# Optimization experiments

Hardware: AMD Instinct MI355X
Metric: run time of the kernel (lower is better)

Reference implementation:

```python
import jax, jax.numpy as jnp
import numpy as np

B, C, H, W = 8, 256, 64, 64


def setup_inputs() -> dict:
    key = jax.random.key(0)
    ks = jax.random.split(key, 8)
    s = 1.0 / np.sqrt(C)
    return {
        "x": jax.random.normal(ks[0], (B, C, H, W), dtype=jnp.float32),
        "Wq": jax.random.normal(ks[1], (C, C), dtype=jnp.float32) * s,
        "bq": jax.random.normal(ks[2], (C,), dtype=jnp.float32) * 0.01,
        "Wk": jax.random.normal(ks[3], (C, C), dtype=jnp.float32) * s,
        "bk": jax.random.normal(ks[4], (C,), dtype=jnp.float32) * 0.01,
        "Wv": jax.random.normal(ks[5], (C, C), dtype=jnp.float32) * s,
        "bv": jax.random.normal(ks[6], (C,), dtype=jnp.float32) * 0.01,
        "gamma": jax.random.normal(ks[7], (1,), dtype=jnp.float32) * 0.1,
    }


def reference(x, Wq, bq, Wk, bk, Wv, bv, gamma):
    b, c, h, w = x.shape
    xf = x.reshape(b, c, h * w)                       # (B, C, N)
    # 1x1 conv == per-pixel linear: out_c = W @ in_c + bias
    q = jnp.einsum('oc,bcn->bon', Wq, xf) + bq[None, :, None]
    k = jnp.einsum('oc,bcn->bon', Wk, xf) + bk[None, :, None]
    v = jnp.einsum('oc,bcn->bon', Wv, xf) + bv[None, :, None]
    # attention_map[b, i, j] = sum_c q[b, c, i] * k[b, c, j]  (no scaling in original)
    scores = jnp.einsum('bci,bcj->bij', q, k)         # (B, N, N)
    attn = jax.nn.softmax(scores, axis=-1)
    # out[b, c, i] = sum_j v[b, c, j] * attn[b, i, j]
    out = jnp.einsum('bcj,bij->bci', v, attn)
    out = out.reshape(b, c, h, w)
    return x + gamma[0] * out
```

## Files before the change

kernel.cpp:

```cpp
#include <hip/hip_runtime.h>

#define BATCH 8
#define CCH 256
#define NPOS 4096
#define LOG2E 1.4426950408889634f

typedef __bf16 bf16x8 __attribute__((ext_vector_type(8)));
typedef float f32x4 __attribute__((ext_vector_type(4)));
typedef int i32x4 __attribute__((ext_vector_type(4)));
typedef int i32x2 __attribute__((ext_vector_type(2)));

typedef const __attribute__((address_space(1))) void GAS;
typedef __attribute__((address_space(3))) void LAS;

#define CFENCE() __asm__ volatile("" ::: "memory")
#define WAIT_VM8()  do { CFENCE(); __builtin_amdgcn_s_waitcnt(0x0F78); CFENCE(); } while (0)
#define WAIT_LGKM0() do { CFENCE(); __builtin_amdgcn_s_waitcnt(0xC07F); CFENCE(); } while (0)
#define BAR_RAW() do { CFENCE(); __builtin_amdgcn_s_barrier(); CFENCE(); } while (0)

__device__ __forceinline__ unsigned short f2bf(float f) {
  unsigned u = __builtin_bit_cast(unsigned, f);
  u += 0x7fffu + ((u >> 16) & 1u);
  return (unsigned short)(u >> 16);
}

__device__ __forceinline__ bf16x8 ld_bf8(const unsigned short* p) {
  i32x4 t = *reinterpret_cast<const i32x4*>(p);
  return __builtin_bit_cast(bf16x8, t);
}

__device__ __forceinline__ float fexp2(float x) {
#if __has_builtin(__builtin_amdgcn_exp2f)
  return __builtin_amdgcn_exp2f(x);
#else
  return __builtin_exp2f(x);
#endif
}

__device__ __forceinline__ unsigned cvtpk(float lo, float hi) {
  unsigned r;
  asm("v_cvt_pk_bf16_f32 %0, %1, %2" : "=v"(r) : "v"(lo), "v"(hi));
  return r;
}

__global__ void cvt_kernel(const float* __restrict__ Wq,
                           const float* __restrict__ Wk,
                           const float* __restrict__ Wv,
                           unsigned short* __restrict__ dst)
{
  const int idx = blockIdx.x * 256 + threadIdx.x;
  const float* src = (idx < 65536) ? Wq : ((idx < 131072) ? Wk : Wv);
  dst[idx] = f2bf(src[idx & 65535]);
}

__global__ __launch_bounds__(256, 3)
void qkv_kernel(const float* __restrict__ x,
                const unsigned short* __restrict__ Wall,
                const float* __restrict__ bq,
                const float* __restrict__ bk,
                const float* __restrict__ bv,
                unsigned short* __restrict__ qT,
                unsigned short* __restrict__ kT,
                unsigned short* __restrict__ vG)
{
  __shared__ __align__(16) unsigned short xT[64 * 264];
  __shared__ __align__(16) unsigned short tbuf[64 * 72];

  const int b   = blockIdx.x;
  const int i0  = blockIdx.y * 64;
  const int tid = threadIdx.x;
  const int w   = tid >> 6;
  const int l   = tid & 63;
  const int n   = l & 15;
  const int q4  = l >> 4;

  {
    const int li = tid & 15;
    const int cg = tid >> 4;
#pragma unroll
    for (int it = 0; it < 16; ++it) {
      const int c = it * 16 + cg;
      f32x4 f = *reinterpret_cast<const f32x4*>(x + ((size_t)b * CCH + c) * NPOS + i0 + li * 4);
#pragma unroll
      for (int e = 0; e < 4; ++e) xT[(li * 4 + e) * 264 + c] = f2bf(f[e]);
    }
  }
  __syncthreads();

  const size_t qbase = (size_t)b * NPOS * CCH;
  bool first = true;

  for (int s = 0; s < 3; ++s) {
    const float* bias = (s == 0) ? bq : (s == 1) ? bk : bv;
    for (int op = 0; op < 4; ++op) {
      const int obase = op * 64;

      const unsigned short* Wp = Wall + s * 65536 + (size_t)(obase + w * 16 + n) * CCH + q4 * 8;
      bf16x8 wfr[8];
#pragma unroll
      for (int kk = 0; kk < 8; ++kk) wfr[kk] = ld_bf8(Wp + kk * 32);

      float bo[4];
#pragma unroll
      for (int r = 0; r < 4; ++r) bo[r] = bias[obase + w * 16 + q4 * 4 + r];

      f32x4 acc[4];
#pragma unroll
      for (int pt = 0; pt < 4; ++pt) {
        acc[pt] = {0.f, 0.f, 0.f, 0.f};
#pragma unroll
        for (int kk = 0; kk < 8; ++kk) {
          bf16x8 bfr = ld_bf8(&xT[(pt * 16 + n) * 264 + kk * 32 + q4 * 8]);
          acc[pt] = __builtin_amdgcn_mfma_f32_16x16x32_bf16(wfr[kk], bfr, acc[pt], 0, 0, 0);
        }
      }

      if (!first) __syncthreads();
      first = false;
      if (s < 2) {
        const float sc = (s == 0) ? LOG2E : 1.0f;
#pragma unroll
        for (int pt = 0; pt < 4; ++pt)
#pragma unroll
          for (int r = 0; r < 4; ++r)
            tbuf[(pt * 16 + n) * 72 + w * 16 + q4 * 4 + r] = f2bf((acc[pt][r] + bo[r]) * sc);
      } else {
#pragma unroll
        for (int pt = 0; pt < 4; ++pt)
#pragma unroll
          for (int r = 0; r < 4; ++r)
            tbuf[(w * 16 + q4 * 4 + r) * 72 + pt * 16 + n] = f2bf(acc[pt][r] + bo[r]);
      }
      __syncthreads();

      if (s < 2) {
        unsigned short* dst = (s == 0 ? qT : kT) + qbase;
#pragma unroll
        for (int it2 = 0; it2 < 2; ++it2) {
          const int idx = it2 * 256 + tid;
          const int pos = idx >> 3, ow = (idx & 7) * 8;
          i32x4 d = *reinterpret_cast<const i32x4*>(&tbuf[pos * 72 + ow]);
          *reinterpret_cast<i32x4*>(&dst[(size_t)(i0 + pos) * CCH + obase + ow]) = d;
        }
      } else {
#pragma unroll
        for (int it2 = 0; it2 < 2; ++it2) {
          const int idx = it2 * 256 + tid;
          const int o = idx >> 3, pw2 = (idx & 7) * 8;
          i32x4 d = *reinterpret_cast<const i32x4*>(&tbuf[o * 72 + pw2]);
          *reinterpret_cast<i32x4*>(&vG[qbase + (size_t)(obase + o) * NPOS + i0 + pw2]) = d;
        }
      }
    }
  }
}

__global__ __launch_bounds__(256, 2)
void attn_kernel(const unsigned short* __restrict__ qT,
                 const unsigned short* __restrict__ kT,
                 const unsigned short* __restrict__ vG,
                 const float* __restrict__ x,
                 const float* __restrict__ gamma,
                 float* __restrict__ out)
{
  __shared__ __align__(16) unsigned short kbuf[2][64 * 256];
  __shared__ __align__(16) unsigned short pbuf[64 * 64];
  __shared__ float stat_lds[64];

  const int b   = blockIdx.x;
  const int i0  = blockIdx.y * 64;
  const int tid = threadIdx.x;
  const int w   = tid >> 6;
  const int l   = tid & 63;
  const int n   = l & 15;
  const int q4  = l >> 4;
  const int nsw = n & 7;

  const unsigned short* qTb = qT + (size_t)b * NPOS * CCH;
  const unsigned short* kTb = kT + (size_t)b * NPOS * CCH;
  const unsigned short* vb  = vG + (size_t)b * NPOS * CCH;

  bf16x8 afr[8];
  {
    const unsigned short* qrow = qTb + (size_t)(i0 + w * 16 + n) * CCH + q4 * 8;
#pragma unroll
    for (int kk = 0; kk < 8; ++kk)
      afr[kk] = ld_bf8(qrow + kk * 32);
  }

  {
#pragma unroll
    for (int it = 0; it < 8; ++it) {
      const int t = w * 8 + it;
      const int j = 2 * t + (l >> 5);
      const int gp = l & 31;
      const int g  = gp ^ (j & 7);
      const unsigned short* src = kTb + (size_t)j * CCH + g * 8;
      unsigned short* dst = &kbuf[0][t * 512];
      __builtin_amdgcn_global_load_lds((GAS*)src, (LAS*)dst, 16, 0, 0);
    }
  }

  f32x4 O[16];
#pragma unroll
  for (int t = 0; t < 16; ++t) O[t] = {0.f, 0.f, 0.f, 0.f};
  float mcur = 64.f;
  float lrow = 0.f;
  float acarry = 1.0f;

  for (int jt = 0; jt < 64; ++jt) {
    const int j0 = jt * 64;
    const unsigned short* kb = kbuf[jt & 1];

    i32x4 vreg[8];
#pragma unroll
    for (int ct = 0; ct < 4; ++ct) {
      const unsigned short* vp = vb + (size_t)(w * 64 + ct * 16 + n) * NPOS + j0 + q4 * 8;
      vreg[ct * 2]     = *reinterpret_cast<const i32x4*>(vp);
      vreg[ct * 2 + 1] = *reinterpret_cast<const i32x4*>(vp + 32);
    }

    WAIT_VM8();
    BAR_RAW();

    f32x4 sacc[4];
    __builtin_amdgcn_s_setprio(1);
#pragma unroll
    for (int nt = 0; nt < 4; ++nt) {
      const unsigned short* krow = kb + (nt * 16 + n) * 256;
      sacc[nt] = {0.f, 0.f, 0.f, 0.f};
#pragma unroll
      for (int kk = 0; kk < 8; ++kk) {
        const int gp = (kk * 4 + q4) ^ nsw;
        bf16x8 bfr = ld_bf8(krow + gp * 8);
        sacc[nt] = __builtin_amdgcn_mfma_f32_16x16x32_bf16(bfr, afr[kk], sacc[nt], 0, 0, 0);
      }
    }
    __builtin_amdgcn_s_setprio(0);

    float tml;
    {
      float a0 = fmaxf(fmaxf(sacc[0][0], sacc[0][1]), fmaxf(sacc[0][2], sacc[0][3]));
      float a1 = fmaxf(fmaxf(sacc[1][0], sacc[1][1]), fmaxf(sacc[1][2], sacc[1][3]));
      float a2 = fmaxf(fmaxf(sacc[2][0], sacc[2][1]), fmaxf(sacc[2][2], sacc[2][3]));
      float a3 = fmaxf(fmaxf(sacc[3][0], sacc[3][1]), fmaxf(sacc[3][2], sacc[3][3]));
      tml = fmaxf(fmaxf(a0, a1), fmaxf(a2, a3));
    }

    float s = 0.f;
#pragma unroll
    for (int nt = 0; nt < 4; ++nt) {
#pragma unroll
      for (int r = 0; r < 4; ++r) {
        const float p = fexp2(sacc[nt][r] - mcur);
        sacc[nt][r] = p;
        s += p;
      }
    }

    {
      const int rowb = (w * 16 + n) * 64;
#pragma unroll
      for (int nt = 0; nt < 4; ++nt) {
        const unsigned lo = cvtpk(sacc[nt][0], sacc[nt][1]);
        const unsigned hi = cvtpk(sacc[nt][2], sacc[nt][3]);
        const int pg = (2 * nt + (q4 >> 1)) ^ nsw;
        i32x2 dv = { (int)lo, (int)hi };
        *reinterpret_cast<i32x2*>(&pbuf[rowb + pg * 8 + (q4 & 1) * 4]) = dv;
      }
    }
    if (q4 == 0) stat_lds[w * 16 + n] = acarry;

    s += __shfl_xor(s, 16);
    s += __shfl_xor(s, 32);
    lrow += s;
    float tm = fmaxf(tml, __shfl_xor(tml, 16));
    tm = fmaxf(tm, __shfl_xor(tm, 32));

    {
      const int j0n = ((jt + 1) & 63) * 64;
      unsigned short* bufn = kbuf[(jt + 1) & 1];
#pragma unroll
      for (int it = 0; it < 8; ++it) {
        const int t = w * 8 + it;
        const int j = 2 * t + (l >> 5);
        const int gp = l & 31;
        const int g  = gp ^ (j & 7);
        const unsigned short* src = kTb + (size_t)(j0n + j) * CCH + g * 8;
        unsigned short* dst = &bufn[t * 512];
        __builtin_amdgcn_global_load_lds((GAS*)src, (LAS*)dst, 16, 0, 0);
      }
    }

    WAIT_LGKM0();
    BAR_RAW();

    {
      const float al0 = stat_lds[n];
      const float al1 = stat_lds[16 + n];
      const float al2 = stat_lds[32 + n];
      const float al3 = stat_lds[48 + n];
      if (al0 + al1 + al2 + al3 != 4.0f) {
        const float als[4] = { al0, al1, al2, al3 };
#pragma unroll
        for (int it = 0; it < 4; ++it) {
          const float al = als[it];
#pragma unroll
          for (int ct = 0; ct < 4; ++ct) {
            f32x4& o = O[ct * 4 + it];
            o[0] *= al; o[1] *= al; o[2] *= al; o[3] *= al;
          }
        }
      }
    }

    bf16x8 pf[8];
#pragma unroll
    for (int it = 0; it < 4; ++it) {
      const int rowb = (it * 16 + n) * 64;
      pf[it * 2 + 0] = ld_bf8(&pbuf[rowb + ((q4 ^ nsw) << 3)]);
      pf[it * 2 + 1] = ld_bf8(&pbuf[rowb + (((4 + q4) ^ nsw) << 3)]);
    }
    __builtin_amdgcn_s_setprio(1);
#pragma unroll
    for (int ct = 0; ct < 4; ++ct) {
      bf16x8 vf0 = __builtin_bit_cast(bf16x8, vreg[ct * 2]);
      bf16x8 vf1 = __builtin_bit_cast(bf16x8, vreg[ct * 2 + 1]);
#pragma unroll
      for (int it = 0; it < 4; ++it) {
        O[ct * 4 + it] = __builtin_amdgcn_mfma_f32_16x16x32_bf16(vf0, pf[it * 2 + 0], O[ct * 4 + it], 0, 0, 0);
        O[ct * 4 + it] = __builtin_amdgcn_mfma_f32_16x16x32_bf16(vf1, pf[it * 2 + 1], O[ct * 4 + it], 0, 0, 0);
      }
    }
    __builtin_amdgcn_s_setprio(0);

    const int upd = tm > mcur + 8.f;
    if (__any(upd)) {
      const float mn = upd ? tm : mcur;
      const float al = fexp2(mcur - mn);
      mcur = mn;
      lrow *= al;
      acarry = al;
    } else {
      acarry = 1.0f;
    }
  }

  __syncthreads();
  if (q4 == 0) stat_lds[w * 16 + n] = acarry / lrow;
  __syncthreads();

  const float g = gamma[0];
#pragma unroll
  for (int it = 0; it < 4; ++it) {
    const float sc = g * stat_lds[it * 16 + n];
    const int ipos = i0 + it * 16 + n;
#pragma unroll
    for (int ct = 0; ct < 4; ++ct) {
#pragma unroll
      for (int r = 0; r < 4; ++r) {
        const int c = w * 64 + ct * 16 + q4 * 4 + r;
        const size_t idx = ((size_t)(b * CCH + c)) * NPOS + ipos;
        out[idx] = x[idx] + sc * O[ct * 4 + it][r];
      }
    }
  }
}

extern "C" void kernel_launch(void* const* d_in, const int* in_sizes, int n_in,
                              void* d_out, int out_size, void* d_ws, size_t ws_size,
                              hipStream_t stream)
{
  const float* x     = (const float*)d_in[0];
  const float* Wq    = (const float*)d_in[1];
  const float* bq    = (const float*)d_in[2];
  const float* Wk    = (const float*)d_in[3];
  const float* bk    = (const float*)d_in[4];
  const float* Wv    = (const float*)d_in[5];
  const float* bv    = (const float*)d_in[6];
  const float* gamma = (const float*)d_in[7];
  float* out = (float*)d_out;

  unsigned short* ws   = (unsigned short*)d_ws;
  unsigned short* Wall = ws;
  unsigned short* qT   = ws + 196608;
  unsigned short* kT   = qT + (size_t)BATCH * NPOS * CCH;
  unsigned short* vG   = kT + (size_t)BATCH * NPOS * CCH;

  cvt_kernel<<<768, 256, 0, stream>>>(Wq, Wk, Wv, Wall);
  qkv_kernel<<<dim3(8, 64), 256, 0, stream>>>(x, Wall, bq, bk, bv, qT, kT, vG);
  attn_kernel<<<dim3(8, 64), 256, 0, stream>>>(qT, kT, vG, x, gamma, out);
}
```

Before: 296.1 us.

## Split QK^T work so each wave computes two query groups over half the keys

Each of the four waves now owns two 16-row query groups and half of the 64-key tile, instead of one query group against all keys. Each K fragment read from LDS feeds two MFMAs, so LDS K reads per MFMA are halved. Partial row sums and maxima are exchanged between wave pairs through a new shared stats array. This costs more VGPRs, since two sets of Q fragments are held, and adds an extra LDS stat exchange. The launch bound is expressed as amdgpu_waves_per_eu(2,2).

```diff
diff --git a/kernel.cpp b/kernel.cpp
--- a/kernel.cpp
+++ b/kernel.cpp
@@ -155,7 +155,7 @@
   }
 }
 
-__global__ __launch_bounds__(256, 2)
+__global__ __launch_bounds__(256) __attribute__((amdgpu_waves_per_eu(2, 2)))
 void attn_kernel(const unsigned short* __restrict__ qT,
                  const unsigned short* __restrict__ kT,
                  const unsigned short* __restrict__ vG,
@@ -166,6 +166,7 @@
   __shared__ __align__(16) unsigned short kbuf[2][64 * 256];
   __shared__ __align__(16) unsigned short pbuf[64 * 64];
   __shared__ float stat_lds[64];
+  __shared__ float sstat[2][2][64];
 
   const int b   = blockIdx.x;
   const int i0  = blockIdx.y * 64;
@@ -175,17 +176,20 @@
   const int n   = l & 15;
   const int q4  = l >> 4;
   const int nsw = n & 7;
+  const int ip  = w >> 1;
+  const int jh  = w & 1;
 
   const unsigned short* qTb = qT + (size_t)b * NPOS * CCH;
   const unsigned short* kTb = kT + (size_t)b * NPOS * CCH;
   const unsigned short* vb  = vG + (size_t)b * NPOS * CCH;
 
-  bf16x8 afr[8];
-  {
-    const unsigned short* qrow = qTb + (size_t)(i0 + w * 16 + n) * CCH + q4 * 8;
+  bf16x8 afr[2][8];
+#pragma unroll
+  for (int ig = 0; ig < 2; ++ig) {
+    const unsigned short* qrow = qTb + (size_t)(i0 + (ip * 2 + ig) * 16 + n) * CCH + q4 * 8;
 #pragma unroll
     for (int kk = 0; kk < 8; ++kk)
-      afr[kk] = ld_bf8(qrow + kk * 32);
+      afr[ig][kk] = ld_bf8(qrow + kk * 32);
   }
 
   {
@@ -204,9 +208,9 @@
   f32x4 O[16];
 #pragma unroll
   for (int t = 0; t < 16; ++t) O[t] = {0.f, 0.f, 0.f, 0.f};
-  float mcur = 64.f;
-  float lrow = 0.f;
-  float acarry = 1.0f;
+  float mcur[2] = {64.f, 64.f};
+  float lrow[2] = {0.f, 0.f};
+  float acarry[2] = {1.0f, 1.0f};
 
   for (int jt = 0; jt < 64; ++jt) {
     const int j0 = jt * 64;
@@ -223,59 +227,73 @@
     WAIT_VM8();
     BAR_RAW();
 
-    f32x4 sacc[4];
+    f32x4 sacc[2][2];
+#pragma unroll
+    for (int nt2 = 0; nt2 < 2; ++nt2)
+#pragma unroll
+      for (int ig = 0; ig < 2; ++ig) sacc[nt2][ig] = {0.f, 0.f, 0.f, 0.f};
     __builtin_amdgcn_s_setprio(1);
 #pragma unroll
-    for (int nt = 0; nt < 4; ++nt) {
-      const unsigned short* krow = kb + (nt * 16 + n) * 256;
-      sacc[nt] = {0.f, 0.f, 0.f, 0.f};
+    for (int nt2 = 0; nt2 < 2; ++nt2) {
+      const unsigned short* krow = kb + (jh * 32 + nt2 * 16 + n) * 256;
 #pragma unroll
       for (int kk = 0; kk < 8; ++kk) {
         const int gp = (kk * 4 + q4) ^ nsw;
-        bf16x8 bfr = ld_bf8(krow + gp * 8);
-        sacc[nt] = __builtin_amdgcn_mfma_f32_16x16x32_bf16(bfr, afr[kk], sacc[nt], 0, 0, 0);
+        bf16x8 kfr = ld_bf8(krow + gp * 8);
+        sacc[nt2][0] = __builtin_amdgcn_mfma_f32_16x16x32_bf16(kfr, afr[0][kk], sacc[nt2][0], 0, 0, 0);
+        sacc[nt2][1] = __builtin_amdgcn_mfma_f32_16x16x32_bf16(kfr, afr[1][kk], sacc[nt2][1], 0, 0, 0);
       }
     }
     __builtin_amdgcn_s_setprio(0);
 
-    float tml;
-    {
-      float a0 = fmaxf(fmaxf(sacc[0][0], sacc[0][1]), fmaxf(sacc[0][2], sacc[0][3]));
-      float a1 = fmaxf(fmaxf(sacc[1][0], sacc[1][1]), fmaxf(sacc[1][2], sacc[1][3]));
-      float a2 = fmaxf(fmaxf(sacc[2][0], sacc[2][1]), fmaxf(sacc[2][2], sacc[2][3]));
-      float a3 = fmaxf(fmaxf(sacc[3][0], sacc[3][1]), fmaxf(sacc[3][2], sacc[3][3]));
-      tml = fmaxf(fmaxf(a0, a1), fmaxf(a2, a3));
-    }
-
-    float s = 0.f;
-#pragma unroll
-    for (int nt = 0; nt < 4; ++nt) {
-#pragma unroll
-      for (int r = 0; r < 4; ++r) {
-        const float p = fexp2(sacc[nt][r] - mcur);
-        sacc[nt][r] = p;
-        s += p;
-      }
-    }
-
-    {
-      const int rowb = (w * 16 + n) * 64;
-#pragma unroll
-      for (int nt = 0; nt < 4; ++nt) {
-        const unsigned lo = cvtpk(sacc[nt][0], sacc[nt][1]);
-        const unsigned hi = cvtpk(sacc[nt][2], sacc[nt][3]);
-        const int pg = (2 * nt + (q4 >> 1)) ^ nsw;
+    float tml[2], s_[2];
+#pragma unroll
+    for (int ig = 0; ig < 2; ++ig) {
+      float a0 = fmaxf(fmaxf(sacc[0][ig][0], sacc[0][ig][1]), fmaxf(sacc[0][ig][2], sacc[0][ig][3]));
+      float a1 = fmaxf(fmaxf(sacc[1][ig][0], sacc[1][ig][1]), fmaxf(sacc[1][ig][2], sacc[1][ig][3]));
+      tml[ig] = fmaxf(a0, a1);
+      float s = 0.f;
+#pragma unroll
+      for (int nt2 = 0; nt2 < 2; ++nt2)
+#pragma unroll
+        for (int r = 0; r < 4; ++r) {
+          const float p = fexp2(sacc[nt2][ig][r] - mcur[ig]);
+          sacc[nt2][ig][r] = p;
+          s += p;
+        }
+      s_[ig] = s;
+    }
+
+#pragma unroll
+    for (int ig = 0; ig < 2; ++ig) {
+      const int rowb = ((ip * 2 + ig) * 16 + n) * 64;
+#pragma unroll
+      for (int nt2 = 0; nt2 < 2; ++nt2) {
+        const unsigned lo = cvtpk(sacc[nt2][ig][0], sacc[nt2][ig][1]);
+        const unsigned hi = cvtpk(sacc[nt2][ig][2], sacc[nt2][ig][3]);
+        const int pg = (jh * 4 + nt2 * 2 + (q4 >> 1)) ^ nsw;
         i32x2 dv = { (int)lo, (int)hi };
         *reinterpret_cast<i32x2*>(&pbuf[rowb + pg * 8 + (q4 & 1) * 4]) = dv;
       }
     }
-    if (q4 == 0) stat_lds[w * 16 + n] = acarry;
-
-    s += __shfl_xor(s, 16);
-    s += __shfl_xor(s, 32);
-    lrow += s;
-    float tm = fmaxf(tml, __shfl_xor(tml, 16));
-    tm = fmaxf(tm, __shfl_xor(tm, 32));
+
+#pragma unroll
+    for (int ig = 0; ig < 2; ++ig) {
+      s_[ig] += __shfl_xor(s_[ig], 16);
+      s_[ig] += __shfl_xor(s_[ig], 32);
+      tml[ig] = fmaxf(tml[ig], __shfl_xor(tml[ig], 16));
+      tml[ig] = fmaxf(tml[ig], __shfl_xor(tml[ig], 32));
+    }
+
+    if (q4 == 0) {
+#pragma unroll
+      for (int ig = 0; ig < 2; ++ig) {
+        const int irow = (ip * 2 + ig) * 16 + n;
+        sstat[jh][0][irow] = s_[ig];
+        sstat[jh][1][irow] = tml[ig];
+        if (jh == 0) stat_lds[irow] = acarry[ig];
+      }
+    }
 
     {
       const int j0n = ((jt + 1) & 63) * 64;
@@ -295,6 +313,14 @@
     WAIT_LGKM0();
     BAR_RAW();
 
+    float sp[2], mp[2];
+#pragma unroll
+    for (int ig = 0; ig < 2; ++ig) {
+      const int irow = (ip * 2 + ig) * 16 + n;
+      sp[ig] = sstat[jh ^ 1][0][irow];
+      mp[ig] = sstat[jh ^ 1][1][irow];
+    }
+
     {
       const float al0 = stat_lds[n];
       const float al1 = stat_lds[16 + n];
@@ -334,20 +360,34 @@
     }
     __builtin_amdgcn_s_setprio(0);
 
-    const int upd = tm > mcur + 8.f;
-    if (__any(upd)) {
-      const float mn = upd ? tm : mcur;
-      const float al = fexp2(mcur - mn);
-      mcur = mn;
-      lrow *= al;
-      acarry = al;
+    const float tm0 = fmaxf(tml[0], mp[0]);
+    const float tm1 = fmaxf(tml[1], mp[1]);
+    lrow[0] += s_[0] + sp[0];
+    lrow[1] += s_[1] + sp[1];
+    const int upd0 = tm0 > mcur[0] + 8.f;
+    const int upd1 = tm1 > mcur[1] + 8.f;
+    if (__any(upd0 | upd1)) {
+      {
+        const float mn = upd0 ? tm0 : mcur[0];
+        const float al = fexp2(mcur[0] - mn);
+        mcur[0] = mn; lrow[0] *= al; acarry[0] = al;
+      }
+      {
+        const float mn = upd1 ? tm1 : mcur[1];
+        const float al = fexp2(mcur[1] - mn);
+        mcur[1] = mn; lrow[1] *= al; acarry[1] = al;
+      }
     } else {
-      acarry = 1.0f;
+      acarry[0] = 1.0f; acarry[1] = 1.0f;
     }
   }
 
   __syncthreads();
-  if (q4 == 0) stat_lds[w * 16 + n] = acarry / lrow;
+  if (q4 == 0 && jh == 0) {
+#pragma unroll
+    for (int ig = 0; ig < 2; ++ig)
+      stat_lds[(ip * 2 + ig) * 16 + n] = acarry[ig] / lrow[ig];
+  }
   __syncthreads();
 
   const float g = gamma[0];
```

Result: slower. 350.6 us (+18.4%).

## Double-buffer QKV staging tile and prefetch next weight fragments

Applied to the files above, without the earlier changes.

Flattens the QKV projection's 12 output phases into one fully unrolled loop. Each phase now prefetches the next phase's weight fragments and biases into registers while the current MFMAs run. The transpose staging buffer becomes double-buffered, so one of the two barriers per phase can be dropped. The aim is to hide global weight-load latency and reduce synchronisation, at the cost of more registers and LDS, which could lower occupancy under the launch bound of 3.

```diff
diff --git a/kernel.cpp b/kernel.cpp
--- a/kernel.cpp
+++ b/kernel.cpp
@@ -64,7 +64,7 @@
                 unsigned short* __restrict__ vG)
 {
   __shared__ __align__(16) unsigned short xT[64 * 264];
-  __shared__ __align__(16) unsigned short tbuf[64 * 72];
+  __shared__ __align__(16) unsigned short tbuf[2][64 * 72];
 
   const int b   = blockIdx.x;
   const int i0  = blockIdx.y * 64;
@@ -88,69 +88,87 @@
   __syncthreads();
 
   const size_t qbase = (size_t)b * NPOS * CCH;
-  bool first = true;
-
-  for (int s = 0; s < 3; ++s) {
-    const float* bias = (s == 0) ? bq : (s == 1) ? bk : bv;
-    for (int op = 0; op < 4; ++op) {
-      const int obase = op * 64;
-
-      const unsigned short* Wp = Wall + s * 65536 + (size_t)(obase + w * 16 + n) * CCH + q4 * 8;
-      bf16x8 wfr[8];
-#pragma unroll
-      for (int kk = 0; kk < 8; ++kk) wfr[kk] = ld_bf8(Wp + kk * 32);
-
-      float bo[4];
-#pragma unroll
-      for (int r = 0; r < 4; ++r) bo[r] = bias[obase + w * 16 + q4 * 4 + r];
-
-      f32x4 acc[4];
-#pragma unroll
-      for (int pt = 0; pt < 4; ++pt) {
-        acc[pt] = {0.f, 0.f, 0.f, 0.f};
-#pragma unroll
-        for (int kk = 0; kk < 8; ++kk) {
-          bf16x8 bfr = ld_bf8(&xT[(pt * 16 + n) * 264 + kk * 32 + q4 * 8]);
-          acc[pt] = __builtin_amdgcn_mfma_f32_16x16x32_bf16(wfr[kk], bfr, acc[pt], 0, 0, 0);
-        }
-      }
-
-      if (!first) __syncthreads();
-      first = false;
-      if (s < 2) {
-        const float sc = (s == 0) ? LOG2E : 1.0f;
-#pragma unroll
-        for (int pt = 0; pt < 4; ++pt)
-#pragma unroll
-          for (int r = 0; r < 4; ++r)
-            tbuf[(pt * 16 + n) * 72 + w * 16 + q4 * 4 + r] = f2bf((acc[pt][r] + bo[r]) * sc);
-      } else {
-#pragma unroll
-        for (int pt = 0; pt < 4; ++pt)
-#pragma unroll
-          for (int r = 0; r < 4; ++r)
-            tbuf[(w * 16 + q4 * 4 + r) * 72 + pt * 16 + n] = f2bf(acc[pt][r] + bo[r]);
-      }
-      __syncthreads();
-
-      if (s < 2) {
-        unsigned short* dst = (s == 0 ? qT : kT) + qbase;
-#pragma unroll
-        for (int it2 = 0; it2 < 2; ++it2) {
-          const int idx = it2 * 256 + tid;
-          const int pos = idx >> 3, ow = (idx & 7) * 8;
-          i32x4 d = *reinterpret_cast<const i32x4*>(&tbuf[pos * 72 + ow]);
-          *reinterpret_cast<i32x4*>(&dst[(size_t)(i0 + pos) * CCH + obase + ow]) = d;
-        }
-      } else {
-#pragma unroll
-        for (int it2 = 0; it2 < 2; ++it2) {
-          const int idx = it2 * 256 + tid;
-          const int o = idx >> 3, pw2 = (idx & 7) * 8;
-          i32x4 d = *reinterpret_cast<const i32x4*>(&tbuf[o * 72 + pw2]);
-          *reinterpret_cast<i32x4*>(&vG[qbase + (size_t)(obase + o) * NPOS + i0 + pw2]) = d;
-        }
-      }
+  const float* const biases[3] = { bq, bk, bv };
+
+  bf16x8 wcur[8];
+  float bcur[4];
+  {
+    const unsigned short* Wp = Wall + (size_t)(w * 16 + n) * CCH + q4 * 8;
+#pragma unroll
+    for (int kk = 0; kk < 8; ++kk) wcur[kk] = ld_bf8(Wp + kk * 32);
+#pragma unroll
+    for (int r = 0; r < 4; ++r) bcur[r] = bq[w * 16 + q4 * 4 + r];
+  }
+
+#pragma unroll
+  for (int ph = 0; ph < 12; ++ph) {
+    const int s = ph >> 2, op = ph & 3, obase = op * 64;
+
+    bf16x8 wnxt[8];
+    float bnxt[4];
+    if (ph < 11) {
+      const int s2 = (ph + 1) >> 2, op2 = (ph + 1) & 3;
+      const unsigned short* Wp =
+          Wall + s2 * 65536 + (size_t)(op2 * 64 + w * 16 + n) * CCH + q4 * 8;
+#pragma unroll
+      for (int kk = 0; kk < 8; ++kk) wnxt[kk] = ld_bf8(Wp + kk * 32);
+      const float* b2 = biases[s2];
+#pragma unroll
+      for (int r = 0; r < 4; ++r) bnxt[r] = b2[op2 * 64 + w * 16 + q4 * 4 + r];
+    }
+
+    f32x4 acc[4];
+#pragma unroll
+    for (int pt = 0; pt < 4; ++pt) {
+      acc[pt] = {0.f, 0.f, 0.f, 0.f};
+#pragma unroll
+      for (int kk = 0; kk < 8; ++kk) {
+        bf16x8 bfr = ld_bf8(&xT[(pt * 16 + n) * 264 + kk * 32 + q4 * 8]);
+        acc[pt] = __builtin_amdgcn_mfma_f32_16x16x32_bf16(wcur[kk], bfr, acc[pt], 0, 0, 0);
+      }
+    }
+
+    unsigned short* tb = tbuf[ph & 1];
+    if (s < 2) {
+      const float sc = (s == 0) ? LOG2E : 1.0f;
+#pragma unroll
+      for (int pt = 0; pt < 4; ++pt)
+#pragma unroll
+        for (int r = 0; r < 4; ++r)
+          tb[(pt * 16 + n) * 72 + w * 16 + q4 * 4 + r] = f2bf((acc[pt][r] + bcur[r]) * sc);
+    } else {
+#pragma unroll
+      for (int pt = 0; pt < 4; ++pt)
+#pragma unroll
+        for (int r = 0; r < 4; ++r)
+          tb[(w * 16 + q4 * 4 + r) * 72 + pt * 16 + n] = f2bf(acc[pt][r] + bcur[r]);
+    }
+    __syncthreads();
+
+    if (s < 2) {
+      unsigned short* dst = (s == 0 ? qT : kT) + qbase;
+#pragma unroll
+      for (int it2 = 0; it2 < 2; ++it2) {
+        const int idx = it2 * 256 + tid;
+        const int pos = idx >> 3, ow = (idx & 7) * 8;
+        i32x4 d = *reinterpret_cast<const i32x4*>(&tb[pos * 72 + ow]);
+        *reinterpret_cast<i32x4*>(&dst[(size_t)(i0 + pos) * CCH + obase + ow]) = d;
+      }
+    } else {
+#pragma unroll
+      for (int it2 = 0; it2 < 2; ++it2) {
+        const int idx = it2 * 256 + tid;
+        const int o = idx >> 3, pw2 = (idx & 7) * 8;
+        i32x4 d = *reinterpret_cast<const i32x4*>(&tb[o * 72 + pw2]);
+        *reinterpret_cast<i32x4*>(&vG[qbase + (size_t)(obase + o) * NPOS + i0 + pw2]) = d;
+      }
+    }
+
+    if (ph < 11) {
+#pragma unroll
+      for (int kk = 0; kk < 8; ++kk) wcur[kk] = wnxt[kk];
+#pragma unroll
+      for (int r = 0; r < 4; ++r) bcur[r] = bnxt[r];
     }
   }
 }
```

New measurement: 292.0 us. Within noise of the previous version (-1.4%).
